# Kernel tuning notes

Hardware: AMD Instinct MI355X
Metric: run time of the kernel (lower is better)

Reference implementation:

```python
import jax, jax.numpy as jnp
import numpy as np

B, S_IMG, S_TXT = 2, 2048, 256
DIM, H, D = 1024, 16, 64
EPS = 1e-6


def _rmsnorm(x, w):
    x32 = x.astype(jnp.float32)
    rms = jnp.sqrt(jnp.mean(x32 * x32, axis=-1, keepdims=True) + EPS)
    return (x32 / rms * w.astype(jnp.float32)).astype(x.dtype)


def _heads(x):  # [B,S,DIM] -> [B,H,S,D]
    b, s, _ = x.shape
    return x.reshape(b, s, H, D).transpose(0, 2, 1, 3)


def setup_inputs() -> dict:
    key = jax.random.key(0)
    ks = jax.random.split(key, 20)
    lin = lambda k: (jax.random.normal(k, (DIM, DIM), jnp.float32) * 0.02,
                     jnp.zeros((DIM,), jnp.float32))
    wq, bq = lin(ks[0]); wk, bk = lin(ks[1]); wv, bv = lin(ks[2])
    waq, baq = lin(ks[3]); wak, bak = lin(ks[4]); wav, bav = lin(ks[5])
    wout, bout = lin(ks[6]); waout, baout = lin(ks[7])
    return {
        "img_hidden": jax.random.normal(ks[8], (B, S_IMG, DIM), jnp.float32),
        "txt_hidden": jax.random.normal(ks[9], (B, S_TXT, DIM), jnp.float32),
        "wq": wq, "bq": bq, "wk": wk, "bk": bk, "wv": wv, "bv": bv,
        "waq": waq, "baq": baq, "wak": wak, "bak": bak, "wav": wav, "bav": bav,
        "wout": wout, "bout": bout, "waout": waout, "baout": baout,
        "gq": jnp.ones((D,), jnp.float32), "gk": jnp.ones((D,), jnp.float32),
        "gaq": jnp.ones((D,), jnp.float32), "gak": jnp.ones((D,), jnp.float32),
    }


def reference(img_hidden, txt_hidden, wq, bq, wk, bk, wv, bv,
              waq, baq, wak, bak, wav, bav, wout, bout, waout, baout,
              gq, gk, gaq, gak):
    batch = img_hidden.shape[0]
    # joint QKV projections (torch Linear: x @ W.T + b)
    q = _heads(img_hidden @ wq.T + bq)
    k = _heads(img_hidden @ wk.T + bk)
    v = _heads(img_hidden @ wv.T + bv)
    aq = _heads(txt_hidden @ waq.T + baq)
    ak = _heads(txt_hidden @ wak.T + bak)
    av = _heads(txt_hidden @ wav.T + bav)
    # per-head RMSNorm on Q/K
    q, k = _rmsnorm(q, gq), _rmsnorm(k, gk)
    aq, ak = _rmsnorm(aq, gaq), _rmsnorm(ak, gak)
    # concat streams along sequence: [B,H,S_img+S_txt,D]
    fq = jnp.concatenate([q, aq], axis=2)
    fk = jnp.concatenate([k, ak], axis=2)
    fv = jnp.concatenate([v, av], axis=2)
    scale = 1.0 / jnp.sqrt(jnp.float32(D))
    attn = jnp.einsum('bhqd,bhkd->bhqk', fq, fk) * scale
    attn = jax.nn.softmax(attn, axis=-1)
    out = jnp.einsum('bhqk,bhkd->bhqd', attn, fv)
    out = out.transpose(0, 2, 1, 3)  # [B,S,H,D]
    s_img = q.shape[2]
    img_out = out[:, :s_img].reshape(batch, s_img, -1)
    txt_out = out[:, s_img:].reshape(batch, aq.shape[2], -1)
    img_out = img_out @ wout.T + bout
    txt_out = txt_out @ waout.T + baout
    return (img_out, txt_out)
```

## Files before the change

### kernel.cpp

```cpp
#include <hip/hip_runtime.h>
#include <stdint.h>

#define BATCH 2
#define SIMG 2048
#define STXT 256
#define STOT 2304
#define DIM 1024
#define NH 16
#define HD 64

typedef unsigned short u16;
typedef __attribute__((ext_vector_type(8))) short bf16x8;
typedef __attribute__((ext_vector_type(4))) float f32x4;
typedef __attribute__((ext_vector_type(2))) uint32_t u32x2;

__device__ __forceinline__ u16 f2bf(float f) {
  union { float f; uint32_t u; } v; v.f = f;
  uint32_t r = (v.u + 0x7FFFu + ((v.u >> 16) & 1u)) >> 16;
  return (u16)r;
}
__device__ __forceinline__ float bf2f(u16 h) {
  union { uint32_t u; float f; } v; v.u = ((uint32_t)h) << 16; return v.f;
}

__device__ __forceinline__ void async_load16(const u16* g, u16* l) {
  __builtin_amdgcn_global_load_lds(
      (const __attribute__((address_space(1))) uint32_t*)g,
      (__attribute__((address_space(3))) uint32_t*)l, 16, 0, 0);
}

__device__ __forceinline__ bf16x8 cvt8(const float* p) {
  const f32x4 a = *(const f32x4*)p;
  const f32x4 b = *(const f32x4*)(p + 4);
  union { bf16x8 v; u16 s[8]; } r;
  r.s[0] = f2bf(a[0]); r.s[1] = f2bf(a[1]); r.s[2] = f2bf(a[2]); r.s[3] = f2bf(a[3]);
  r.s[4] = f2bf(b[0]); r.s[5] = f2bf(b[1]); r.s[6] = f2bf(b[2]); r.s[7] = f2bf(b[3]);
  return r.v;
}

__device__ __forceinline__ float gain_at(const u16* g, int d) {
  if (g[0] == 0) return ((const float*)g)[d];
  return bf2f(g[d]);
}

__global__ __launch_bounds__(256)
void cvt_all(const float* s0, const float* s1, const float* s2, const float* s3,
             const float* s4, const float* s5, const float* s6, const float* s7,
             const float* s8, const float* s9,
             u16* d0, u16* d1, u16* d2, u16* d3, u16* d4,
             u16* d5, u16* d6, u16* d7, u16* d8, u16* d9)
{
  const int z = blockIdx.z;
  const float* srcs[10] = {s0,s1,s2,s3,s4,s5,s6,s7,s8,s9};
  u16* dsts[10] = {d0,d1,d2,d3,d4,d5,d6,d7,d8,d9};
  const int ns[10] = {BATCH*SIMG*DIM, BATCH*STXT*DIM, DIM*DIM, DIM*DIM, DIM*DIM,
                      DIM*DIM, DIM*DIM, DIM*DIM, DIM*DIM, DIM*DIM};
  const long i = ((long)blockIdx.x * 256 + threadIdx.x) * 8;
  if (i >= ns[z]) return;
  *(bf16x8*)(dsts[z] + i) = cvt8(srcs[z] + i);
}

template<int MODE, int TN>
__global__ __launch_bounds__(256)
void gemm_bt(const u16* __restrict__ Ai, const u16* __restrict__ At,
             const u16* __restrict__ Wi0, const u16* __restrict__ Wi1, const u16* __restrict__ Wi2,
             const u16* __restrict__ Wt0, const u16* __restrict__ Wt1, const u16* __restrict__ Wt2,
             const float* __restrict__ bi0, const float* __restrict__ bi1, const float* __restrict__ bi2,
             const float* __restrict__ bt0, const float* __restrict__ bt1, const float* __restrict__ bt2,
             void* __restrict__ Di0, void* __restrict__ Di1, void* __restrict__ Di2,
             void* __restrict__ Dt0, void* __restrict__ Dt1, void* __restrict__ Dt2,
             const u16* __restrict__ gi0, const u16* __restrict__ gi1,
             const u16* __restrict__ gt0, const u16* __restrict__ gt1,
             int ysplit)
{
  constexpr int GX = DIM / TN;
  constexpr int GXL = (TN == 128) ? 3 : 4;
  constexpr int CHUNK = (36 * GX) / 8;
  constexpr int WN = TN / 64;
  constexpr int WMROWS = 128 / (4 / WN);
  constexpr int MT = WMROWS / 16;

  const int z = blockIdx.z;
  const int wg = (int)blockIdx.x + GX * (int)blockIdx.y;
  const int swz = (wg & 7) * CHUNK + (wg >> 3);
  const int bx = swz & (GX - 1);
  const int by = swz >> GXL;

  const bool txt = by >= ysplit;
  const int yy = txt ? (by - ysplit) : by;

  const u16* A = txt ? At : Ai;
  const u16* W      = txt ? ((z == 0) ? Wt0 : ((z == 1) ? Wt1 : Wt2))
                          : ((z == 0) ? Wi0 : ((z == 1) ? Wi1 : Wi2));
  const float* bias = txt ? ((z == 0) ? bt0 : ((z == 1) ? bt1 : bt2))
                          : ((z == 0) ? bi0 : ((z == 1) ? bi1 : bi2));
  void* Dst         = txt ? ((z == 0) ? Dt0 : ((z == 1) ? Dt1 : Dt2))
                          : ((z == 0) ? Di0 : ((z == 1) ? Di1 : Di2));

  const int slog = txt ? 8 : 11;
  const int smask = (1 << slog) - 1;
  const int batch_rows = (MODE == 0) ? (txt ? STXT : SIMG) : STOT;
  const int src_off    = (MODE == 0) ? 0 : (txt ? SIMG : 0);
  const int dst_off    = (MODE == 0) ? (txt ? SIMG : 0) : 0;

  const int m0 = yy * 128;
  const int n0 = bx * TN;
  const int tid = threadIdx.x;
  const int lane = tid & 63;
  const int w = tid >> 6;
  const int wm = (WN == 2) ? (w >> 1) : w;
  const int wn = (WN == 2) ? (w & 1) : 0;
  const int l15 = lane & 15, quad = lane >> 4;

  __shared__ __attribute__((aligned(16))) u16 As[2][128 * 32];
  __shared__ __attribute__((aligned(16))) u16 Bs[2][TN * 32];

  const int srow = tid >> 2;
  const int scol = (tid & 3) * 8;

  long aoff0, aoff1;
  {
    int m = m0 + srow;
    aoff0 = ((long)(m >> slog) * batch_rows + src_off + (m & smask)) * DIM + scol;
    m = m0 + 64 + srow;
    aoff1 = ((long)(m >> slog) * batch_rows + src_off + (m & smask)) * DIM + scol;
  }
  const u16* wp0 = W + (long)(n0 + srow) * DIM + scol;
  const u16* wp1 = W + (long)(n0 + 64 + srow) * DIM + scol;

  const f32x4 fzero = {0.f, 0.f, 0.f, 0.f};
  f32x4 acc[MT][4];
  #pragma unroll
  for (int i = 0; i < MT; ++i)
    #pragma unroll
    for (int j = 0; j < 4; ++j) acc[i][j] = fzero;

  auto stage = [&](int bf, int kt) {
    async_load16(A + aoff0 + kt, &As[bf][tid * 8]);
    async_load16(A + aoff1 + kt, &As[bf][2048 + tid * 8]);
    async_load16(wp0 + kt, &Bs[bf][tid * 8]);
    if constexpr (TN == 128) async_load16(wp1 + kt, &Bs[bf][2048 + tid * 8]);
  };

  stage(0, 0);
  int cur = 0;

  for (int kt = 0; kt < DIM; kt += 32) {
    __syncthreads();
    if (kt + 32 < DIM) stage(cur ^ 1, kt + 32);
    const u16* Asc = As[cur];
    const u16* Bsc = Bs[cur];

    bf16x8 af[MT], bfg[4];
    #pragma unroll
    for (int mt = 0; mt < MT; ++mt)
      af[mt] = *(const bf16x8*)(Asc + (wm * WMROWS + mt * 16 + l15) * 32 + quad * 8);
    #pragma unroll
    for (int nt = 0; nt < 4; ++nt)
      bfg[nt] = *(const bf16x8*)(Bsc + (wn * 64 + nt * 16 + l15) * 32 + quad * 8);
    #pragma unroll
    for (int mt = 0; mt < MT; ++mt)
      #pragma unroll
      for (int nt = 0; nt < 4; ++nt)
        acc[mt][nt] = __builtin_amdgcn_mfma_f32_16x16x32_bf16(af[mt], bfg[nt], acc[mt][nt], 0, 0, 0);
    cur ^= 1;
  }

  if (MODE == 0 && z != 2) {
    const u16* gsel = txt ? ((z == 0) ? gt0 : gt1) : ((z == 0) ? gi0 : gi1);
    float gv[4];
    #pragma unroll
    for (int nt = 0; nt < 4; ++nt) gv[nt] = gain_at(gsel, nt * 16 + l15);
    #pragma unroll
    for (int mt = 0; mt < MT; ++mt) {
      float vals[4][4];
      #pragma unroll
      for (int nt = 0; nt < 4; ++nt) {
        const float bb = bias[n0 + wn * 64 + nt * 16 + l15];
        #pragma unroll
        for (int r = 0; r < 4; ++r) vals[nt][r] = acc[mt][nt][r] + bb;
      }
      #pragma unroll
      for (int r = 0; r < 4; ++r) {
        float ss = vals[0][r] * vals[0][r] + vals[1][r] * vals[1][r]
                 + vals[2][r] * vals[2][r] + vals[3][r] * vals[3][r];
        #pragma unroll
        for (int d = 1; d < 16; d <<= 1) ss += __shfl_xor(ss, d, 64);
        const float scn = rsqrtf(ss * (1.0f / 64.0f) + 1e-6f);
        const int grow = m0 + wm * WMROWS + mt * 16 + quad * 4 + r;
        const int b = grow >> slog;
        const int sl = grow & smask;
        #pragma unroll
        for (int nt = 0; nt < 4; ++nt) {
          const int gcol = n0 + wn * 64 + nt * 16 + l15;
          const int h = gcol >> 6, d2 = gcol & 63;
          const long idx = (((long)(b * NH + h)) * STOT + dst_off + sl) * HD + d2;
          ((u16*)Dst)[idx] = f2bf(vals[nt][r] * scn * gv[nt]);
        }
      }
    }
  } else {
    #pragma unroll
    for (int mt = 0; mt < MT; ++mt) {
      #pragma unroll
      for (int nt = 0; nt < 4; ++nt) {
        const int gcol = n0 + wn * 64 + nt * 16 + l15;
        const float bb = bias[gcol];
        const f32x4 v = acc[mt][nt];
        #pragma unroll
        for (int r = 0; r < 4; ++r) {
          const int grow = m0 + wm * WMROWS + mt * 16 + quad * 4 + r;
          const float val = v[r] + bb;
          if (MODE == 0) {
            const int b = grow >> slog;
            const int sl = grow & smask;
            const int h = gcol >> 6, d = gcol & 63;
            const long idx = (((long)(b * NH + h)) * HD + d) * STOT + dst_off + sl;
            ((u16*)Dst)[idx] = f2bf(val);
          } else {
            ((float*)Dst)[(long)grow * DIM + gcol] = val;
          }
        }
      }
    }
  }
}

__global__ __launch_bounds__(256)
void flash_attn_split(const u16* __restrict__ fq, const u16* __restrict__ fk,
                      const u16* __restrict__ fvT,
                      u16* __restrict__ p0, u16* __restrict__ p1,
                      float* __restrict__ l0, float* __restrict__ l1)
{
  const int qt = blockIdx.x;
  const int bh = blockIdx.y;
  const int z = blockIdx.z;
  u16* pout = z ? p1 : p0;
  float* lout = z ? l1 : l0;
  const int it0 = z * (STOT / 128);

  const int tid = threadIdx.x;
  const int lane = tid & 63;
  const int w = tid >> 6;
  const int l15 = lane & 15, quad = lane >> 4;
  const int x7 = l15 & 7;
  const long base = (long)bh * STOT * HD;
  const int b = bh >> 4, h = bh & 15;

  __shared__ __attribute__((aligned(16))) u16 Ks[64 * 64];
  __shared__ __attribute__((aligned(16))) u16 Vt[64 * 64];
  __shared__ __attribute__((aligned(16))) u16 Ps[64 * 72];

  bf16x8 aq[2];
  #pragma unroll
  for (int ks = 0; ks < 2; ++ks)
    aq[ks] = *(const bf16x8*)(fq + base +
        (long)(qt * 64 + w * 16 + l15) * 64 + ks * 32 + quad * 8);

  const f32x4 fzero = {0.f, 0.f, 0.f, 0.f};
  f32x4 Oc[4];
  float lsum = 0.f;
  #pragma unroll
  for (int nt = 0; nt < 4; ++nt) Oc[nt] = fzero;

  const float C1 = 0.18033688011112042f;
  const float C8 = 11.541560327111707f;

  const int srow = tid >> 3;
  const int sseg = (tid & 7) ^ (srow & 7);
  const int sr2 = srow + 32;
  u16* const pwr = Ps + (w * 16 + l15) * 72 + quad * 4;

  for (int it = it0; it < it0 + STOT / 128; ++it) {
    __syncthreads();
    const u16* ksrc = fk + base + (long)it * 64 * 64;
    async_load16(ksrc + srow * 64 + sseg * 8, Ks + tid * 8);
    async_load16(ksrc + sr2 * 64 + sseg * 8, Ks + 2048 + tid * 8);
    const u16* vsrc = fvT + base + (long)it * 64;
    async_load16(vsrc + (long)srow * STOT + sseg * 8, Vt + tid * 8);
    async_load16(vsrc + (long)sr2 * STOT + sseg * 8, Vt + 2048 + tid * 8);
    __syncthreads();

    f32x4 sc[4];
    #pragma unroll
    for (int nt = 0; nt < 4; ++nt) sc[nt] = fzero;
    #pragma unroll
    for (int ks = 0; ks < 2; ++ks) {
      bf16x8 bk[4];
      #pragma unroll
      for (int nt = 0; nt < 4; ++nt)
        bk[nt] = *(const bf16x8*)(Ks + (nt * 16 + l15) * 64 + (((ks * 4 + quad) ^ x7) * 8));
      #pragma unroll
      for (int nt = 0; nt < 4; ++nt)
        sc[nt] = __builtin_amdgcn_mfma_f32_16x16x32_bf16(bk[nt], aq[ks], sc[nt], 0, 0, 0);
    }

    #pragma unroll
    for (int nt = 0; nt < 4; ++nt) {
      const uint32_t u0 = __float_as_uint(exp2f(sc[nt][0] * C1 - C8));
      const uint32_t u1 = __float_as_uint(exp2f(sc[nt][1] * C1 - C8));
      const uint32_t u2 = __float_as_uint(exp2f(sc[nt][2] * C1 - C8));
      const uint32_t u3 = __float_as_uint(exp2f(sc[nt][3] * C1 - C8));
      u32x2 pk;
      pk[0] = (u0 >> 16) | (u1 & 0xFFFF0000u);
      pk[1] = (u2 >> 16) | (u3 & 0xFFFF0000u);
      *(u32x2*)(pwr + nt * 16) = pk;
      lsum += __uint_as_float(u0 & 0xFFFF0000u) + __uint_as_float(u1 & 0xFFFF0000u)
            + __uint_as_float(u2 & 0xFFFF0000u) + __uint_as_float(u3 & 0xFFFF0000u);
    }

    #pragma unroll
    for (int ks = 0; ks < 2; ++ks) {
      const bf16x8 ap = *(const bf16x8*)(Ps + (w * 16 + l15) * 72 + ks * 32 + quad * 8);
      bf16x8 bv[4];
      #pragma unroll
      for (int nt = 0; nt < 4; ++nt)
        bv[nt] = *(const bf16x8*)(Vt + (nt * 16 + l15) * 64 + (((ks * 4 + quad) ^ x7) * 8));
      #pragma unroll
      for (int nt = 0; nt < 4; ++nt)
        Oc[nt] = __builtin_amdgcn_mfma_f32_16x16x32_bf16(ap, bv[nt], Oc[nt], 0, 0, 0);
    }
  }

  float ls = lsum;
  ls += __shfl_xor(ls, 16, 64);
  ls += __shfl_xor(ls, 32, 64);
  if (quad == 0)
    lout[(long)bh * STOT + qt * 64 + w * 16 + l15] = ls;

  #pragma unroll
  for (int nt = 0; nt < 4; ++nt) {
    const int d = nt * 16 + l15;
    #pragma unroll
    for (int r = 0; r < 4; ++r) {
      const int q = qt * 64 + w * 16 + quad * 4 + r;
      pout[(((long)b * STOT + q) * NH + h) * HD + d] = f2bf(Oc[nt][r]);
    }
  }
}

__global__ __launch_bounds__(256)
void attn_combine(const u16* __restrict__ p1, const float* __restrict__ l0,
                  const float* __restrict__ l1, u16* __restrict__ p0io)
{
  const long i = ((long)blockIdx.x * 256 + threadIdx.x) * 8;
  const long rem = i >> 6;
  const int h = (int)(rem & 15);
  const long bq = rem >> 4;
  const int b = bq >= STOT;
  const int q = (int)(bq - (long)b * STOT);
  const long li = ((long)(b * NH + h)) * STOT + q;
  const float inv = 1.0f / (l0[li] + l1[li]);
  union { bf16x8 v; u16 s[8]; } a, c, o;
  a.v = *(const bf16x8*)(p0io + i);
  c.v = *(const bf16x8*)(p1 + i);
  #pragma unroll
  for (int j = 0; j < 8; ++j)
    o.s[j] = f2bf((bf2f(a.s[j]) + bf2f(c.s[j])) * inv);
  *(bf16x8*)(p0io + i) = o.v;
}

extern "C" void kernel_launch(void* const* d_in, const int* in_sizes, int n_in,
                              void* d_out, int out_size, void* d_ws, size_t ws_size,
                              hipStream_t stream)
{
  int iImg = 0, iTxt = 1;
  if (in_sizes[0] < in_sizes[1]) { iImg = 1; iTxt = 0; }
  const float* img  = (const float*)d_in[iImg];
  const float* txt  = (const float*)d_in[iTxt];
  const float* wq   = (const float*)d_in[2];
  const float* bq   = (const float*)d_in[3];
  const float* wk   = (const float*)d_in[4];
  const float* bk   = (const float*)d_in[5];
  const float* wv   = (const float*)d_in[6];
  const float* bv   = (const float*)d_in[7];
  const float* waq  = (const float*)d_in[8];
  const float* baq  = (const float*)d_in[9];
  const float* wak  = (const float*)d_in[10];
  const float* bak  = (const float*)d_in[11];
  const float* wav  = (const float*)d_in[12];
  const float* bav  = (const float*)d_in[13];
  const float* wout = (const float*)d_in[14];
  const float* bout = (const float*)d_in[15];
  const float* waout= (const float*)d_in[16];
  const float* baout= (const float*)d_in[17];
  const u16* gq   = (const u16*)d_in[18];
  const u16* gk   = (const u16*)d_in[19];
  const u16* gaq  = (const u16*)d_in[20];
  const u16* gak  = (const u16*)d_in[21];

  const long NE = (long)BATCH * NH * STOT * HD;
  const long NIMG = (long)BATCH * SIMG * DIM;
  const long NW = (long)DIM * DIM;

  u16* fq  = (u16*)d_ws;
  u16* fk  = fq + NE;
  u16* fvT = fk + NE;
  u16* imgb = fvT + NE;
  u16* txtb = imgb + NIMG;
  u16* aob  = imgb;
  u16* woutb  = imgb + NE;
  u16* waoutb = woutb + NW;
  float* lsum0 = (float*)(waoutb + NW);
  float* lsum1 = lsum0 + (long)BATCH * NH * STOT;
  u16* qw = (u16*)d_out;
  u16* wqb = qw, *wkb = qw + NW, *wvb = qw + 2*NW;
  u16* waqb = qw + 3*NW, *wakb = qw + 4*NW, *wavb = qw + 5*NW;
  u16* p1 = (u16*)d_out;
  float* out = (float*)d_out;
  float* outt = out + (long)BATCH * SIMG * DIM;

  const dim3 blk(256, 1, 1);

  hipLaunchKernelGGL(cvt_all, dim3((int)(NIMG / 2048), 1, 10), blk, 0, stream,
                     img, txt, wq, wk, wv, waq, wak, wav, wout, waout,
                     imgb, txtb, wqb, wkb, wvb, waqb, wakb, wavb, woutb, waoutb);
  hipLaunchKernelGGL((gemm_bt<0, 128>), dim3(8, 36, 3), blk, 0, stream,
                     imgb, txtb, wqb, wkb, wvb, waqb, wakb, wavb,
                     bq, bk, bv, baq, bak, bav,
                     fq, fk, fvT, fq, fk, fvT,
                     gq, gk, gaq, gak, 32);
  hipLaunchKernelGGL(flash_attn_split, dim3(STOT / 64, BATCH * NH, 2), blk, 0, stream,
                     fq, fk, fvT, aob, p1, lsum0, lsum1);
  hipLaunchKernelGGL(attn_combine, dim3((int)(NE / 2048)), blk, 0, stream,
                     p1, lsum0, lsum1, aob);
  hipLaunchKernelGGL((gemm_bt<1, 64>), dim3(16, 36, 1), blk, 0, stream,
                     aob, aob, woutb, woutb, woutb, waoutb, waoutb, waoutb,
                     bout, bout, bout, baout, baout, baout,
                     out, out, out, outt, outt, outt,
                     nullptr, nullptr, nullptr, nullptr, 32);
}
```

Measured before the change: 305.0 us.

## Triple-buffer GEMM loads with vmcnt waits; swizzle P tile and add setprio in attention

```diff
diff --git a/kernel.cpp b/kernel.cpp
--- a/kernel.cpp
+++ b/kernel.cpp
@@ -112,8 +112,8 @@
   const int wn = (WN == 2) ? (w & 1) : 0;
   const int l15 = lane & 15, quad = lane >> 4;
 
-  __shared__ __attribute__((aligned(16))) u16 As[2][128 * 32];
-  __shared__ __attribute__((aligned(16))) u16 Bs[2][TN * 32];
+  __shared__ __attribute__((aligned(16))) u16 As[3][128 * 32];
+  __shared__ __attribute__((aligned(16))) u16 Bs[3][TN * 32];
 
   const int srow = tid >> 2;
   const int scol = (tid & 3) * 8;
@@ -143,14 +143,21 @@
   };
 
   stage(0, 0);
-  int cur = 0;
+  stage(1, 32);
+  int rd = 0, wr = 2;
 
   for (int kt = 0; kt < DIM; kt += 32) {
-    __syncthreads();
-    if (kt + 32 < DIM) stage(cur ^ 1, kt + 32);
-    const u16* Asc = As[cur];
-    const u16* Bsc = Bs[cur];
-
+    if (kt + 32 < DIM) {
+      if constexpr (TN == 128) asm volatile("s_waitcnt vmcnt(4)" ::: "memory");
+      else                     asm volatile("s_waitcnt vmcnt(3)" ::: "memory");
+    } else {
+      asm volatile("s_waitcnt vmcnt(0)" ::: "memory");
+    }
+    __builtin_amdgcn_s_barrier();
+    asm volatile("" ::: "memory");
+
+    const u16* Asc = As[rd];
+    const u16* Bsc = Bs[rd];
     bf16x8 af[MT], bfg[4];
     #pragma unroll
     for (int mt = 0; mt < MT; ++mt)
@@ -163,7 +170,10 @@
       #pragma unroll
       for (int nt = 0; nt < 4; ++nt)
         acc[mt][nt] = __builtin_amdgcn_mfma_f32_16x16x32_bf16(af[mt], bfg[nt], acc[mt][nt], 0, 0, 0);
-    cur ^= 1;
+
+    if (kt + 64 < DIM) stage(wr, kt + 64);
+    rd = (rd == 2) ? 0 : rd + 1;
+    wr = (wr == 2) ? 0 : wr + 1;
   }
 
   if (MODE == 0 && z != 2) {
@@ -249,7 +259,7 @@
 
   __shared__ __attribute__((aligned(16))) u16 Ks[64 * 64];
   __shared__ __attribute__((aligned(16))) u16 Vt[64 * 64];
-  __shared__ __attribute__((aligned(16))) u16 Ps[64 * 72];
+  __shared__ __attribute__((aligned(16))) u16 Ps[64 * 64];
 
   bf16x8 aq[2];
   #pragma unroll
@@ -269,7 +279,7 @@
   const int srow = tid >> 3;
   const int sseg = (tid & 7) ^ (srow & 7);
   const int sr2 = srow + 32;
-  u16* const pwr = Ps + (w * 16 + l15) * 72 + quad * 4;
+  u16* const prow_base = Ps + (w * 16 + l15) * 64;
 
   for (int it = it0; it < it0 + STOT / 128; ++it) {
     __syncthreads();
@@ -284,6 +294,7 @@
     f32x4 sc[4];
     #pragma unroll
     for (int nt = 0; nt < 4; ++nt) sc[nt] = fzero;
+    __builtin_amdgcn_s_setprio(1);
     #pragma unroll
     for (int ks = 0; ks < 2; ++ks) {
       bf16x8 bk[4];
@@ -294,6 +305,7 @@
       for (int nt = 0; nt < 4; ++nt)
         sc[nt] = __builtin_amdgcn_mfma_f32_16x16x32_bf16(bk[nt], aq[ks], sc[nt], 0, 0, 0);
     }
+    __builtin_amdgcn_s_setprio(0);
 
     #pragma unroll
     for (int nt = 0; nt < 4; ++nt) {
@@ -304,14 +316,16 @@
       u32x2 pk;
       pk[0] = (u0 >> 16) | (u1 & 0xFFFF0000u);
       pk[1] = (u2 >> 16) | (u3 & 0xFFFF0000u);
-      *(u32x2*)(pwr + nt * 16) = pk;
+      const int wslot = (((nt * 2 + (quad >> 1)) ^ x7) * 8) + ((quad & 1) * 4);
+      *(u32x2*)(prow_base + wslot) = pk;
       lsum += __uint_as_float(u0 & 0xFFFF0000u) + __uint_as_float(u1 & 0xFFFF0000u)
             + __uint_as_float(u2 & 0xFFFF0000u) + __uint_as_float(u3 & 0xFFFF0000u);
     }
 
+    __builtin_amdgcn_s_setprio(1);
     #pragma unroll
     for (int ks = 0; ks < 2; ++ks) {
-      const bf16x8 ap = *(const bf16x8*)(Ps + (w * 16 + l15) * 72 + ks * 32 + quad * 8);
+      const bf16x8 ap = *(const bf16x8*)(prow_base + (((ks * 4 + quad) ^ x7) * 8));
       bf16x8 bv[4];
       #pragma unroll
       for (int nt = 0; nt < 4; ++nt)
@@ -320,6 +334,7 @@
       for (int nt = 0; nt < 4; ++nt)
         Oc[nt] = __builtin_amdgcn_mfma_f32_16x16x32_bf16(ap, bv[nt], Oc[nt], 0, 0, 0);
     }
+    __builtin_amdgcn_s_setprio(0);
   }
 
   float ls = lsum;
```

New measurement: 297.3 us. 1.03x faster.
